# Kernel tuning notes

Hardware: AMD Instinct MI355X
Metric: run time of the kernel (lower is better)

## Reference

```python
import jax, jax.numpy as jnp
import numpy as np

MAX_RES = 5.0  # max_residue_magnitude
DG = 16       # deform_groups
KH = KW = 3
K = KH * KW
PAD = 1
STRIDE = 1
DIL = 1


def conv3x3(x, w, b):
    y = jax.lax.conv_general_dilated(
        x, w, window_strides=(1, 1), padding='SAME',
        dimension_numbers=('NCHW', 'OIHW', 'NCHW'))
    return y + b[None, :, None, None]


def lrelu(x):
    return jnp.where(x >= 0, x, 0.1 * x)


def deform_conv2d(x, offset, mask, weight, bias):
    # x: [B,C,H,W]; offset: [B,2*DG*K,Ho,Wo]; mask: [B,DG*K,Ho,Wo]
    B, C, H, W = x.shape
    Cout = weight.shape[0]
    Ho = (H + 2 * PAD - DIL * (KH - 1) - 1) // STRIDE + 1
    Wo = (W + 2 * PAD - DIL * (KW - 1) - 1) // STRIDE + 1
    Cg = C // DG

    # torchvision layout: offset channel = g*(2*K) + 2*k + {0:y, 1:x}
    off = offset.reshape(B, DG, K, 2, Ho, Wo)
    oy, ox = off[:, :, :, 0], off[:, :, :, 1]           # [B,DG,K,Ho,Wo]
    msk = mask.reshape(B, DG, K, Ho, Wo)

    ki = DIL * (jnp.arange(K) // KW)                    # [K] kernel row offsets
    kj = DIL * (jnp.arange(K) % KW)
    base_y = STRIDE * jnp.arange(Ho) - PAD              # [Ho]
    base_x = STRIDE * jnp.arange(Wo) - PAD              # [Wo]
    py = base_y[None, None, None, :, None] + ki[None, None, :, None, None] + oy
    px = base_x[None, None, None, None, :] + kj[None, None, :, None, None] + ox

    xg = x.reshape(B, DG, Cg, H * W)

    y0 = jnp.floor(py)
    x0 = jnp.floor(px)
    wy1 = py - y0
    wx1 = px - x0

    def corner(iy, ix, w_c):
        valid = ((iy >= 0) & (iy <= H - 1) & (ix >= 0) & (ix <= W - 1)).astype(x.dtype)
        iyc = jnp.clip(iy, 0, H - 1).astype(jnp.int32)
        ixc = jnp.clip(ix, 0, W - 1).astype(jnp.int32)
        idx = (iyc * W + ixc).reshape(B, DG, 1, K * Ho * Wo)
        g = jnp.take_along_axis(
            xg, jnp.broadcast_to(idx, (B, DG, Cg, K * Ho * Wo)), axis=3)
        g = g.reshape(B, DG, Cg, K, Ho, Wo)
        return g * (w_c * valid)[:, :, None]

    val = (corner(y0, x0, (1 - wy1) * (1 - wx1))
           + corner(y0, x0 + 1, (1 - wy1) * wx1)
           + corner(y0 + 1, x0, wy1 * (1 - wx1))
           + corner(y0 + 1, x0 + 1, wy1 * wx1))

    val = val * msk[:, :, None]                          # modulation
    val = val.reshape(B, C, K, Ho, Wo)                   # columns
    out = jnp.einsum('bckhw,ock->bohw', val, weight.reshape(Cout, C, K))
    return out + bias[None, :, None, None]


def setup_inputs() -> dict:
    key = jax.random.key(0)
    ks = jax.random.split(key, 12)
    B, H, W = 1, 192, 192
    inp = {
        'x':    jax.random.normal(ks[0], (B, 128, H, W), jnp.float32),
        'cond': jax.random.normal(ks[1], (B, 192, H, W), jnp.float32),
        'weight': jax.random.normal(ks[2], (64, 128, 3, 3), jnp.float32) * 0.03,
        'bias':   jax.random.normal(ks[3], (64,), jnp.float32) * 0.01,
        'w1': jax.random.normal(ks[4], (64, 192, 3, 3), jnp.float32) * 0.03,
        'b1': jax.random.normal(ks[5], (64,), jnp.float32) * 0.01,
        'w2': jax.random.normal(ks[6], (64, 64, 3, 3), jnp.float32) * 0.05,
        'b2': jax.random.normal(ks[7], (64,), jnp.float32) * 0.01,
        'w3': jax.random.normal(ks[8], (64, 64, 3, 3), jnp.float32) * 0.05,
        'b3': jax.random.normal(ks[9], (64,), jnp.float32) * 0.01,
        'w4': jax.random.normal(ks[10], (432, 64, 3, 3), jnp.float32) * 0.05,
        'b4': jax.random.normal(ks[11], (432,), jnp.float32) * 0.01,
    }
    return inp


def reference(x, cond, weight, bias, w1, b1, w2, b2, w3, b3, w4, b4):
    h = lrelu(conv3x3(cond, w1, b1))
    h = lrelu(conv3x3(h, w2, b2))
    h = lrelu(conv3x3(h, w3, b3))
    out = conv3x3(h, w4, b4)                       # [B, 27*DG, H, W]
    offset, mask = out[:, :18 * DG], out[:, 18 * DG:]
    offset = MAX_RES * jnp.tanh(offset)
    mask = jax.nn.sigmoid(mask)
    return deform_conv2d(x, offset, mask, weight, bias)
```

## Files before the change

kernel.cpp:

```cpp
#include <hip/hip_runtime.h>
#include <hip/hip_bf16.h>
#include <math.h>

#define IMG_H 192
#define IMG_W 192
#define NPIX (IMG_H * IMG_W)
#define PADW 194
#define PPIX (PADW * PADW)
#define PH 208
#define PW 208

typedef _Float16 h8 __attribute__((ext_vector_type(8)));
typedef _Float16 h4 __attribute__((ext_vector_type(4)));
typedef float f32x4 __attribute__((ext_vector_type(4)));

__device__ __forceinline__ float act_tanh5(float x) {
    const float t = __expf(2.f * x);
    return 5.f * (t - 1.f) / (t + 1.f);
}
__device__ __forceinline__ float act_sig(float x) {
    return 1.f / (1.f + __expf(-x));
}

typedef __attribute__((address_space(1))) const unsigned int GU32;
typedef __attribute__((address_space(3))) unsigned int LU32;
__device__ __forceinline__ void cp16(const void* g, void* l) {
    __builtin_amdgcn_global_load_lds((GU32*)g, (LU32*)l, 16, 0, 0);
}

__global__ __launch_bounds__(256) void cond_pack_k(
    const float* __restrict__ src, _Float16* __restrict__ dst)
{
    const int y = blockIdx.x;
    const int c = blockIdx.y;
    const int x = threadIdx.x;
    if (x >= PADW) return;
    const bool inb = (y >= 1 && y <= IMG_H && x >= 1 && x <= IMG_W);
    h8 v[4];
#pragma unroll
    for (int j = 0; j < 32; j++)
        ((_Float16*)v)[j] = inb
            ? (_Float16)src[(size_t)(c * 32 + j) * NPIX + (y - 1) * IMG_W + (x - 1)]
            : (_Float16)0.f;
    h8* d = (h8*)&dst[((size_t)c * PPIX + (size_t)y * PADW + x) * 32];
    d[0] = v[0]; d[1] = v[1]; d[2] = v[2]; d[3] = v[3];
}

template<int CIN, int COP, int COUT>
__device__ __forceinline__ void pack_body(
    int bx, const float* __restrict__ src, _Float16* __restrict__ dst)
{
    const int chunk = bx / 9, k = bx % 9;
    for (int i = threadIdx.x; i < COP * 32; i += 256) {
        const int co = i >> 5, cil = i & 31;
        float v = 0.f;
        if (co < COUT)
            v = src[((size_t)(co * CIN + chunk * 32 + cil)) * 9 + k];
        dst[(size_t)bx * COP * 32 + i] = (_Float16)v;
    }
}

__global__ __launch_bounds__(256) void pack_all_w_k(
    const float* __restrict__ w1, const float* __restrict__ w2,
    const float* __restrict__ w3, const float* __restrict__ w4,
    _Float16* __restrict__ wp1, _Float16* __restrict__ wp2,
    _Float16* __restrict__ wp3, _Float16* __restrict__ wp4)
{
    const int b = blockIdx.x;
    if      (b < 54) pack_body<192, 64, 64>(b, w1, wp1);
    else if (b < 72) pack_body<64, 64, 64>(b - 54, w2, wp2);
    else if (b < 90) pack_body<64, 64, 64>(b - 72, w3, wp3);
    else             pack_body<64, 448, 432>(b - 90, w4, wp4);
}

__global__ __launch_bounds__(192) void xg_pack_k(
    const float* __restrict__ x, _Float16* __restrict__ xg)
{
    const int y  = blockIdx.x;
    const int dg = blockIdx.y;
    const int xc = threadIdx.x;
    h8 v;
#pragma unroll
    for (int chl = 0; chl < 8; chl++)
        v[chl] = (_Float16)x[(size_t)(dg * 8 + chl) * NPIX + y * IMG_W + xc];
    *(h8*)&xg[(((size_t)dg * PH + y + 6) * PW + xc + 6) * 8] = v;
}

__global__ __launch_bounds__(256) void wdg_pack_k(
    const float* __restrict__ w, _Float16* __restrict__ wdg)
{
    const int i = blockIdx.x * 256 + threadIdx.x;
    if (i >= 16 * 64 * 96) return;
    const int ks = i % 96;
    const int rest = i / 96;
    const int co = rest % 64;
    const int dg = rest / 64;
    const int k = ks >> 3, chl = ks & 7;
    float v = 0.f;
    if (ks < 72)
        v = w[((size_t)co * 128 + dg * 8 + chl) * 9 + k];
    wdg[i] = (_Float16)v;
}

template<int CHUNKS, int ACT, int COP, int T8>
__global__ __launch_bounds__(256) void conv_lds_k(
    const _Float16* __restrict__ in,
    const _Float16* __restrict__ wpk,
    const float* __restrict__ bias,
    _Float16* __restrict__ out)
{
    constexpr int HALO = T8 ? 10 : 18;
    constexpr int NF   = T8 ? 1 : 4;
    constexpr int TDIM = T8 ? 24 : 12;
    constexpr int TSZ  = T8 ? 8 : 16;
    constexpr int INU  = HALO * HALO * 4;
    constexpr int ROWU = HALO * 4;

    __shared__ _Float16 in_lds[HALO * HALO * 32];
    __shared__ _Float16 w_lds[9 * 64 * 32];

    const int t    = threadIdx.x;
    const int lane = t & 63;
    const int wv   = __builtin_amdgcn_readfirstlane(t >> 6);
    const int col  = lane & 15;
    const int quad = lane >> 4;
    const int bx   = blockIdx.x;
    const int tx0  = (bx % TDIM) * TSZ;
    const int ty0  = (bx / TDIM) * TSZ;
    const int cobase = blockIdx.y * 64;

    f32x4 acc[4][NF];
#pragma unroll
    for (int m = 0; m < 4; m++)
#pragma unroll
        for (int s = 0; s < NF; s++) {
            f32x4 z = {0.f, 0.f, 0.f, 0.f};
            acc[m][s] = z;
        }

    for (int c = 0; c < CHUNKS; c++) {
        __syncthreads();
        {
            const char* gbase = (const char*)in + (size_t)c * PPIX * 64;
            char* lbase = (char*)in_lds + (size_t)wv * 64 * 16;
#pragma unroll
            for (int i = 0; i < (INU + 255) / 256; i++) {
                const int j = t + i * 256;
                if (j < INU) {
                    const int row = j / ROWU;
                    const int u   = j - row * ROWU;
                    cp16(gbase + ((size_t)(ty0 + row) * PADW + tx0) * 64 + u * 16,
                         lbase + (size_t)i * 256 * 16);
                }
            }
        }
        {
            const char* gw = (const char*)wpk
                + ((size_t)(c * 9) * COP + cobase) * 64 + t * 16;
            char* lw = (char*)w_lds + (size_t)wv * 64 * 16;
#pragma unroll
            for (int k = 0; k < 9; k++)
                cp16(gw + (size_t)k * COP * 64, lw + k * 4096);
        }
        __syncthreads();

#pragma unroll
        for (int k = 0; k < 9; k++) {
            const int ky = k / 3, kx = k % 3;
            h8 af[4];
#pragma unroll
            for (int m = 0; m < 4; m++)
                af[m] = *(const h8*)&w_lds[(k * 64 + m * 16 + col) * 32 + quad * 8];
            h8 bf[NF];
            if (T8) {
                bf[0] = *(const h8*)&in_lds[
                    ((2 * wv + (col >> 3) + ky) * HALO + (col & 7) + kx) * 32 + quad * 8];
            } else {
#pragma unroll
                for (int s = 0; s < NF; s++)
                    bf[s] = *(const h8*)&in_lds[
                        ((4 * wv + s + ky) * HALO + col + kx) * 32 + quad * 8];
            }
#pragma unroll
            for (int m = 0; m < 4; m++)
#pragma unroll
                for (int s = 0; s < NF; s++)
                    acc[m][s] = __builtin_amdgcn_mfma_f32_16x16x32_f16(
                        af[m], bf[s], acc[m][s], 0, 0, 0);
        }
    }

#pragma unroll
    for (int m = 0; m < 4; m++) {
#pragma unroll
        for (int s = 0; s < NF; s++) {
            int gy, gx;
            if (T8) { gy = ty0 + 2 * wv + (col >> 3); gx = tx0 + (col & 7); }
            else    { gy = ty0 + 4 * wv + s;          gx = tx0 + col; }
            const int ca = cobase + m * 16 + quad * 4;
            if (ACT == 1) {
                h4 st;
#pragma unroll
                for (int r = 0; r < 4; r++) {
                    float v = acc[m][s][r] + bias[ca + r];
                    st[r] = (_Float16)((v >= 0.f) ? v : 0.1f * v);
                }
                *(h4*)&out[((size_t)(ca >> 5) * PPIX + (size_t)(gy + 1) * PADW + (gx + 1)) * 32
                           + (ca & 31)] = st;
            } else {
#pragma unroll
                for (int r = 0; r < 4; r++) {
                    const int co = ca + r;
                    if (co < 432)
                        out[(size_t)co * NPIX + (size_t)gy * IMG_W + gx] =
                            (_Float16)(acc[m][s][r] + bias[co]);
                }
            }
        }
    }
}

__global__ __launch_bounds__(256) void deform_mfma_k(
    const _Float16* __restrict__ xg,
    const _Float16* __restrict__ od,
    const _Float16* __restrict__ wdg,
    const float* __restrict__ bias,
    float* __restrict__ out)
{
    __shared__ __align__(16) _Float16 val4[4][32][104];

    const int t    = threadIdx.x;
    const int lane = t & 63;
    const int wv   = __builtin_amdgcn_readfirstlane(t >> 6);
    const int col  = lane & 15;
    const int quad = lane >> 4;
    const int bx   = blockIdx.x;
    const int gy   = bx / 6;
    const int gx0  = (bx % 6) * 32;
    const int pixrow = gy * IMG_W + gx0;

    for (int i = t; i < 4 * 32 * 4; i += 256) {
        const int dgl = i >> 7;
        const int r   = i & 127;
        const int px  = r >> 2;
        const int j   = r & 3;
        h8 z = {0, 0, 0, 0, 0, 0, 0, 0};
        *(h8*)&val4[dgl][px][72 + 8 * j] = z;
    }

    f32x4 acc[2];
    {
        f32x4 z = {0.f, 0.f, 0.f, 0.f};
        acc[0] = z; acc[1] = z;
    }

    for (int dq = 0; dq < 4; dq++) {
        __syncthreads();
        for (int idx = t; idx < 1152; idx += 256) {
            const int pxl  = idx & 31;
            const int rest = idx >> 5;
            const int k    = rest % 9;
            const int dgl  = rest / 9;
            const int dg   = dq * 4 + dgl;
            const int kc   = dg * 9 + k;
            const int pix  = pixrow + pxl;
            const float oy = act_tanh5((float)od[(size_t)(2 * kc) * NPIX + pix]);
            const float ox = act_tanh5((float)od[(size_t)(2 * kc + 1) * NPIX + pix]);
            const float m  = act_sig((float)od[(size_t)(288 + kc) * NPIX + pix]);
            const float py  = (float)(gy - 1 + k / 3) + oy;
            const float pxx = (float)(gx0 + pxl - 1 + k % 3) + ox;
            const float y0 = floorf(py), x0 = floorf(pxx);
            const float fy = py - y0, fx = pxx - x0;
            const int iy = (int)y0 + 6, ix = (int)x0 + 6;
            const _Float16* p = xg + (((size_t)dg * PH + iy) * PW + ix) * 8;
            const h8 c00 = *(const h8*)p;
            const h8 c01 = *(const h8*)(p + 8);
            const h8 c10 = *(const h8*)(p + PW * 8);
            const h8 c11 = *(const h8*)(p + PW * 8 + 8);
            const float ey = 1.f - fy, ex = 1.f - fx;
            const _Float16 s00 = (_Float16)(ey * ex * m);
            const _Float16 s01 = (_Float16)(ey * fx * m);
            const _Float16 s10 = (_Float16)(fy * ex * m);
            const _Float16 s11 = (_Float16)(fy * fx * m);
            const h8 v = c00 * s00 + c01 * s01 + c10 * s10 + c11 * s11;
            *(h8*)&val4[dgl][pxl][k * 8] = v;
        }
        __syncthreads();

#pragma unroll
        for (int dgl = 0; dgl < 4; dgl++) {
            const int dg = dq * 4 + dgl;
            const _Float16* wbase = wdg + ((size_t)dg * 64 + wv * 16 + col) * 96;
#pragma unroll
            for (int ks = 0; ks < 3; ks++) {
                const h8 a  = *(const h8*)(wbase + ks * 32 + quad * 8);
                const h8 b0 = *(const h8*)&val4[dgl][col][ks * 32 + quad * 8];
                const h8 b1 = *(const h8*)&val4[dgl][16 + col][ks * 32 + quad * 8];
                acc[0] = __builtin_amdgcn_mfma_f32_16x16x32_f16(a, b0, acc[0], 0, 0, 0);
                acc[1] = __builtin_amdgcn_mfma_f32_16x16x32_f16(a, b1, acc[1], 0, 0, 0);
            }
        }
    }

    const int co = wv * 16 + quad * 4;
#pragma unroll
    for (int n = 0; n < 2; n++) {
        const int gx = gx0 + n * 16 + col;
#pragma unroll
        for (int r = 0; r < 4; r++)
            out[(size_t)(co + r) * NPIX + gy * IMG_W + gx] = acc[n][r] + bias[co + r];
    }
}

extern "C" void kernel_launch(void* const* d_in, const int* in_sizes, int n_in,
                              void* d_out, int out_size, void* d_ws, size_t ws_size,
                              hipStream_t stream) {
    (void)in_sizes; (void)n_in; (void)out_size; (void)ws_size;

    const float* x      = (const float*)d_in[0];
    const float* cond   = (const float*)d_in[1];
    const float* weight = (const float*)d_in[2];
    const float* bias   = (const float*)d_in[3];
    const float* w1     = (const float*)d_in[4];
    const float* b1     = (const float*)d_in[5];
    const float* w2     = (const float*)d_in[6];
    const float* b2     = (const float*)d_in[7];
    const float* w3     = (const float*)d_in[8];
    const float* b3     = (const float*)d_in[9];
    const float* w4     = (const float*)d_in[10];
    const float* b4     = (const float*)d_in[11];
    float* out = (float*)d_out;

    char* ws = (char*)d_ws;
    size_t off = 0;
    auto take = [&](size_t bytes) -> char* {
        char* p = ws + off;
        off = (off + bytes + 255) & ~(size_t)255;
        return p;
    };
    _Float16* act_cond = (_Float16*)take((size_t)6 * PPIX * 32 * 2);
    _Float16* pb_all   = (_Float16*)take((size_t)3 * 2 * PPIX * 32 * 2);
    _Float16* pb1 = pb_all;
    _Float16* pb2 = pb1 + (size_t)2 * PPIX * 32;
    _Float16* pb3 = pb2 + (size_t)2 * PPIX * 32;
    _Float16* od  = (_Float16*)take((size_t)432 * NPIX * 2);
    _Float16* wp1 = (_Float16*)take((size_t)54 * 64 * 32 * 2);
    _Float16* wp2 = (_Float16*)take((size_t)18 * 64 * 32 * 2);
    _Float16* wp3 = (_Float16*)take((size_t)18 * 64 * 32 * 2);
    _Float16* wp4 = (_Float16*)take((size_t)18 * 448 * 32 * 2);
    _Float16* xg  = (_Float16*)take((size_t)16 * PH * PW * 8 * 2);
    _Float16* wdg = (_Float16*)take((size_t)16 * 64 * 96 * 2);

    hipMemsetAsync(pb_all, 0, (size_t)3 * 2 * PPIX * 32 * 2, stream);
    hipMemsetAsync(xg,     0, (size_t)16 * PH * PW * 8 * 2, stream);

    hipLaunchKernelGGL(cond_pack_k, dim3(PADW, 6), dim3(256), 0, stream, cond, act_cond);
    hipLaunchKernelGGL(pack_all_w_k, dim3(108), dim3(256), 0, stream,
                       w1, w2, w3, w4, wp1, wp2, wp3, wp4);
    hipLaunchKernelGGL(xg_pack_k,  dim3(192, 16), dim3(192), 0, stream, x, xg);
    hipLaunchKernelGGL(wdg_pack_k, dim3((16 * 64 * 96 + 255) / 256), dim3(256), 0, stream, weight, wdg);

    hipLaunchKernelGGL((conv_lds_k<6, 1, 64, 1>),  dim3(576, 1), dim3(256), 0, stream, act_cond, wp1, b1, pb1);
    hipLaunchKernelGGL((conv_lds_k<2, 1, 64, 1>),  dim3(576, 1), dim3(256), 0, stream, pb1, wp2, b2, pb2);
    hipLaunchKernelGGL((conv_lds_k<2, 1, 64, 1>),  dim3(576, 1), dim3(256), 0, stream, pb2, wp3, b3, pb3);
    hipLaunchKernelGGL((conv_lds_k<2, 2, 448, 0>), dim3(144, 7), dim3(256), 0, stream, pb3, wp4, b4, od);
    hipLaunchKernelGGL(deform_mfma_k, dim3(1152), dim3(256), 0, stream, xg, od, wdg, bias, out);
}
```

Baseline: 263.2 us.

## Split deform conv over deform-group halves with atomic accumulation and interleaved offset layout

The deform kernel now runs on a 2-D grid, with each block handling half of the deform groups. Partial results are combined with float atomicAdd into an output zeroed by an added memset. The offset conv stores y/x offset pairs interleaved as half2 so the deform kernel reads them with one load. The sampling loop is unrolled with a fixed trip count and launch bounds request higher occupancy. The cost is doubled output traffic through atomics, an extra memset, and a nondeterministic order of summation.

Result: no change. 266.2 us (+1.1%).

```diff
diff --git a/kernel.cpp b/kernel.cpp
--- a/kernel.cpp
+++ b/kernel.cpp
@@ -12,6 +12,7 @@
 
 typedef _Float16 h8 __attribute__((ext_vector_type(8)));
 typedef _Float16 h4 __attribute__((ext_vector_type(4)));
+typedef _Float16 h2 __attribute__((ext_vector_type(2)));
 typedef float f32x4 __attribute__((ext_vector_type(4)));
 
 __device__ __forceinline__ float act_tanh5(float x) {
@@ -208,19 +209,30 @@
                 *(h4*)&out[((size_t)(ca >> 5) * PPIX + (size_t)(gy + 1) * PADW + (gx + 1)) * 32
                            + (ca & 31)] = st;
             } else {
-#pragma unroll
-                for (int r = 0; r < 4; r++) {
-                    const int co = ca + r;
-                    if (co < 432)
-                        out[(size_t)co * NPIX + (size_t)gy * IMG_W + gx] =
-                            (_Float16)(acc[m][s][r] + bias[co]);
+                const int pix = gy * IMG_W + gx;
+#pragma unroll
+                for (int pr = 0; pr < 2; pr++) {
+                    const int co0 = ca + 2 * pr;
+                    if (co0 < 288) {
+                        h2 st;
+                        st[0] = (_Float16)(acc[m][s][2 * pr]     + bias[co0]);
+                        st[1] = (_Float16)(acc[m][s][2 * pr + 1] + bias[co0 + 1]);
+                        *(h2*)&out[((size_t)(co0 >> 1) * NPIX + pix) * 2] = st;
+                    } else if (co0 < 432) {
+#pragma unroll
+                        for (int j = 0; j < 2; j++) {
+                            const int co = co0 + j;
+                            out[(size_t)288 * NPIX + (size_t)(co - 288) * NPIX + pix] =
+                                (_Float16)(acc[m][s][2 * pr + j] + bias[co]);
+                        }
+                    }
                 }
             }
         }
     }
 }
 
-__global__ __launch_bounds__(256) void deform_mfma_k(
+__global__ __launch_bounds__(256, 6) void deform_mfma_k(
     const _Float16* __restrict__ xg,
     const _Float16* __restrict__ od,
     const _Float16* __restrict__ wdg,
@@ -235,9 +247,12 @@
     const int col  = lane & 15;
     const int quad = lane >> 4;
     const int bx   = blockIdx.x;
+    const int dqh  = blockIdx.y;
     const int gy   = bx / 6;
     const int gx0  = (bx % 6) * 32;
     const int pixrow = gy * IMG_W + gx0;
+
+    const _Float16* msk = od + (size_t)288 * NPIX;
 
     for (int i = t; i < 4 * 32 * 4; i += 256) {
         const int dgl = i >> 7;
@@ -254,36 +269,42 @@
         acc[0] = z; acc[1] = z;
     }
 
-    for (int dq = 0; dq < 4; dq++) {
+    for (int ph = 0; ph < 2; ph++) {
+        const int dq = dqh * 2 + ph;
         __syncthreads();
-        for (int idx = t; idx < 1152; idx += 256) {
-            const int pxl  = idx & 31;
-            const int rest = idx >> 5;
-            const int k    = rest % 9;
-            const int dgl  = rest / 9;
-            const int dg   = dq * 4 + dgl;
-            const int kc   = dg * 9 + k;
-            const int pix  = pixrow + pxl;
-            const float oy = act_tanh5((float)od[(size_t)(2 * kc) * NPIX + pix]);
-            const float ox = act_tanh5((float)od[(size_t)(2 * kc + 1) * NPIX + pix]);
-            const float m  = act_sig((float)od[(size_t)(288 + kc) * NPIX + pix]);
-            const float py  = (float)(gy - 1 + k / 3) + oy;
-            const float pxx = (float)(gx0 + pxl - 1 + k % 3) + ox;
-            const float y0 = floorf(py), x0 = floorf(pxx);
-            const float fy = py - y0, fx = pxx - x0;
-            const int iy = (int)y0 + 6, ix = (int)x0 + 6;
-            const _Float16* p = xg + (((size_t)dg * PH + iy) * PW + ix) * 8;
-            const h8 c00 = *(const h8*)p;
-            const h8 c01 = *(const h8*)(p + 8);
-            const h8 c10 = *(const h8*)(p + PW * 8);
-            const h8 c11 = *(const h8*)(p + PW * 8 + 8);
-            const float ey = 1.f - fy, ex = 1.f - fx;
-            const _Float16 s00 = (_Float16)(ey * ex * m);
-            const _Float16 s01 = (_Float16)(ey * fx * m);
-            const _Float16 s10 = (_Float16)(fy * ex * m);
-            const _Float16 s11 = (_Float16)(fy * fx * m);
-            const h8 v = c00 * s00 + c01 * s01 + c10 * s10 + c11 * s11;
-            *(h8*)&val4[dgl][pxl][k * 8] = v;
+#pragma unroll
+        for (int it = 0; it < 5; it++) {
+            const int idx = t + it * 256;
+            if (it < 4 || idx < 1152) {
+                const int pxl  = idx & 31;
+                const int rest = idx >> 5;
+                const int k    = rest % 9;
+                const int dgl  = rest / 9;
+                const int dg   = dq * 4 + dgl;
+                const int kc   = dg * 9 + k;
+                const int pix  = pixrow + pxl;
+                const h2 pr = *(const h2*)&od[((size_t)kc * NPIX + pix) * 2];
+                const float oy = act_tanh5((float)pr[0]);
+                const float ox = act_tanh5((float)pr[1]);
+                const float m  = act_sig((float)msk[(size_t)kc * NPIX + pix]);
+                const float py  = (float)(gy - 1 + k / 3) + oy;
+                const float pxx = (float)(gx0 + pxl - 1 + k % 3) + ox;
+                const float y0 = floorf(py), x0 = floorf(pxx);
+                const float fy = py - y0, fx = pxx - x0;
+                const int iy = (int)y0 + 6, ix = (int)x0 + 6;
+                const _Float16* p = xg + (((size_t)dg * PH + iy) * PW + ix) * 8;
+                const h8 c00 = *(const h8*)p;
+                const h8 c01 = *(const h8*)(p + 8);
+                const h8 c10 = *(const h8*)(p + PW * 8);
+                const h8 c11 = *(const h8*)(p + PW * 8 + 8);
+                const float ey = 1.f - fy, ex = 1.f - fx;
+                const _Float16 s00 = (_Float16)(ey * ex * m);
+                const _Float16 s01 = (_Float16)(ey * fx * m);
+                const _Float16 s10 = (_Float16)(fy * ex * m);
+                const _Float16 s11 = (_Float16)(fy * fx * m);
+                const h8 v = c00 * s00 + c01 * s01 + c10 * s10 + c11 * s11;
+                *(h8*)&val4[dgl][pxl][k * 8] = v;
+            }
         }
         __syncthreads();
 
@@ -307,15 +328,17 @@
     for (int n = 0; n < 2; n++) {
         const int gx = gx0 + n * 16 + col;
 #pragma unroll
-        for (int r = 0; r < 4; r++)
-            out[(size_t)(co + r) * NPIX + gy * IMG_W + gx] = acc[n][r] + bias[co + r];
+        for (int r = 0; r < 4; r++) {
+            float v = acc[n][r] + (dqh == 0 ? bias[co + r] : 0.f);
+            atomicAdd(&out[(size_t)(co + r) * NPIX + gy * IMG_W + gx], v);
+        }
     }
 }
 
 extern "C" void kernel_launch(void* const* d_in, const int* in_sizes, int n_in,
                               void* d_out, int out_size, void* d_ws, size_t ws_size,
                               hipStream_t stream) {
-    (void)in_sizes; (void)n_in; (void)out_size; (void)ws_size;
+    (void)in_sizes; (void)n_in; (void)ws_size;
 
     const float* x      = (const float*)d_in[0];
     const float* cond   = (const float*)d_in[1];
@@ -353,6 +376,7 @@
 
     hipMemsetAsync(pb_all, 0, (size_t)3 * 2 * PPIX * 32 * 2, stream);
     hipMemsetAsync(xg,     0, (size_t)16 * PH * PW * 8 * 2, stream);
+    hipMemsetAsync(out,    0, (size_t)out_size * 4, stream);
 
     hipLaunchKernelGGL(cond_pack_k, dim3(PADW, 6), dim3(256), 0, stream, cond, act_cond);
     hipLaunchKernelGGL(pack_all_w_k, dim3(108), dim3(256), 0, stream,
@@ -364,5 +388,5 @@
     hipLaunchKernelGGL((conv_lds_k<2, 1, 64, 1>),  dim3(576, 1), dim3(256), 0, stream, pb1, wp2, b2, pb2);
     hipLaunchKernelGGL((conv_lds_k<2, 1, 64, 1>),  dim3(576, 1), dim3(256), 0, stream, pb2, wp3, b3, pb3);
     hipLaunchKernelGGL((conv_lds_k<2, 2, 448, 0>), dim3(144, 7), dim3(256), 0, stream, pb3, wp4, b4, od);
-    hipLaunchKernelGGL(deform_mfma_k, dim3(1152), dim3(256), 0, stream, xg, od, wdg, bias, out);
-}
+    hipLaunchKernelGGL(deform_mfma_k, dim3(1152, 2), dim3(256), 0, stream, xg, od, wdg, bias, out);
+}
```
